# Kernel tuning notes

Hardware: AMD Instinct MI355X
Metric: run time of the kernel (lower is better)

The kernel has to match this reference:

```python
import jax, jax.numpy as jnp
import numpy as np

Lx, Ly, D, B = 6, 6, 3, 16
SIGMA = 0.5  # keeps the 36-tensor contraction magnitude in fp32 range


def _slice_config(T, s):
    # T: [Lx, Ly, D,D,D,D, 2,2,2,2,2]; bond axes (u,d,l,r), phys axes (self, up, down, left, right)
    sg = s.reshape(Lx, Ly)
    sp = jnp.pad(sg, 1)  # out-of-grid neighbors -> index 0
    ix, iy = jnp.meshgrid(jnp.arange(Lx), jnp.arange(Ly), indexing='ij')
    p = sg
    pu = sp[ix, iy + 1]      # neighbor (x-1, y)
    pd = sp[ix + 2, iy + 1]  # neighbor (x+1, y)
    pl = sp[ix + 1, iy]      # neighbor (x, y-1)
    pr = sp[ix + 1, iy + 2]  # neighbor (x, y+1)
    # advanced indexing: result [Lx, Ly, D, D, D, D] with bond axes (u, d, l, r)
    return T[ix, iy, :, :, :, :, p, pu, pd, pl, pr]


def _amplitude(T, s):
    # exact boundary contraction from ymin (no truncation), equals full .contract()
    A = _slice_config(T, s)            # [Lx, Ly, u, d, l, r]
    Bnd = A[:, 0, :, :, 0, :]          # cap dangling left bonds: [Lx, u, d, r]
    for y in range(1, Ly):
        C = A[:, y]                    # [Lx, u, d, l, r]
        Bnd = jnp.einsum('xabl,xudlr->xaubdr', Bnd, C)
        Bnd = Bnd.reshape(Lx, Bnd.shape[1] * Bnd.shape[2],
                          Bnd.shape[3] * Bnd.shape[4], D)
    M = Bnd[:, :, :, 0]                # cap dangling right bonds: [Lx, chi, chi]
    v = M[0, 0]                        # cap top boundary bond (index 0 of product bond)
    for xx in range(1, Lx):
        v = v @ M[xx]                  # vector-matrix chain down the boundary MPS
    return v[0]                        # cap bottom boundary bond


def setup_inputs() -> dict:
    key = jax.random.key(0)
    kT, kx = jax.random.split(key)
    T = jax.random.normal(kT, (Lx, Ly, D, D, D, D, 2, 2, 2, 2, 2), dtype=jnp.float32) * SIGMA
    x = jax.random.randint(kx, (B, Lx * Ly), 0, 2, dtype=jnp.int32)
    return {"x": x, "T": T}


def reference(x, T):
    # batched amplitudes: [B]
    return jax.vmap(lambda s: _amplitude(T, s))(x)
```

## Files before the change

kernel.cpp:

```cpp
#include <hip/hip_runtime.h>


constexpr int SITE_STRIDE = 81 * 32;

__global__ __launch_bounds__(512)
void peps_amp_kernel(const int* __restrict__ xs, const float* __restrict__ T,
                     float* __restrict__ out) {
    __shared__ float A[36 * 81];
    __shared__ float Vsh[2][729];
    __shared__ float Wsh[2][2][2187];
    __shared__ float red[8];
    __shared__ int sg[36];
    __shared__ int sidx[36];

    const int b = blockIdx.x;
    const int t = threadIdx.x;
    const int half = t >> 8;
    const int lt = t & 255;

    if (t < 36) sg[t] = xs[b * 36 + t];
    __syncthreads();
    if (t < 36) {
        const int i = t / 6, j = t % 6;
        const int p  = sg[t];
        const int pu = (i > 0) ? sg[t - 6] : 0;
        const int pd = (i < 5) ? sg[t + 6] : 0;
        const int pl = (j > 0) ? sg[t - 1] : 0;
        const int pr = (j < 5) ? sg[t + 1] : 0;
        sidx[t] = (((p * 2 + pu) * 2 + pd) * 2 + pl) * 2 + pr;
    }
    __syncthreads();
    for (int idx = t; idx < 36 * 81; idx += 512) {
        const int site = idx / 81;
        const int perm = idx - site * 81;
        A[idx] = T[site * SITE_STRIDE + perm * 32 + sidx[site]];
    }
    __syncthreads();

    float* V  = Vsh[half];
    float* Wa = Wsh[half][0];
    float* Wb = Wsh[half][1];
    const int SS = half ? 9 : 27;
    const int SO = half ? 27 : 9;

    {
        const float* Arow = &A[(half ? 30 : 0) * 81];
        for (int k = lt; k < 729; k += 256) {
            int c[6];
            c[0] = k / 243;
            c[1] = (k / 81) % 3;
            c[2] = (k / 27) % 3;
            c[3] = (k / 9) % 3;
            c[4] = (k / 3) % 3;
            c[5] = k % 3;
            float v0 = Arow[c[0] * SO + 0];
            float v1 = Arow[c[0] * SO + 1];
            float v2 = Arow[c[0] * SO + 2];
            #pragma unroll
            for (int y = 1; y <= 4; ++y) {
                const float* Ay = Arow + y * 81 + c[y] * SO;
                const float n0 = v0 * Ay[0] + v1 * Ay[3] + v2 * Ay[6];
                const float n1 = v0 * Ay[1] + v1 * Ay[4] + v2 * Ay[7];
                const float n2 = v0 * Ay[2] + v1 * Ay[5] + v2 * Ay[8];
                v0 = n0; v1 = n1; v2 = n2;
            }
            const float* A5 = Arow + 5 * 81 + c[5] * SO;
            V[k] = v0 * A5[0] + v1 * A5[3] + v2 * A5[6];
        }
    }
    __syncthreads();

    for (int cc = 0; cc < 2; ++cc) {
        const int xc = half ? (4 - cc) : (1 + cc);
        const float* Arow = &A[xc * 6 * 81];

        if (lt < 243) {
            const float v0 = V[lt], v1 = V[243 + lt], v2 = V[486 + lt];
            const float* A0 = Arow;
            #pragma unroll
            for (int o = 0; o < 3; ++o)
                #pragma unroll
                for (int r = 0; r < 3; ++r) {
                    Wa[(o * 3 + r) * 243 + lt] =
                        v0 * A0[o * SO + r] +
                        v1 * A0[SS + o * SO + r] +
                        v2 * A0[2 * SS + o * SO + r];
                }
        }
        __syncthreads();

        int cur = 0;
        int P = 81;
        #pragma unroll
        for (int y = 1; y <= 4; ++y) {
            const float* Ay = Arow + y * 81;
            const float* Wp = cur ? Wb : Wa;
            float* Wn = cur ? Wa : Wb;
            if (lt < 243) {
                const int dc = lt / P;
                const int ur = lt - dc * P;
                float wv[3][3];
                #pragma unroll
                for (int l = 0; l < 3; ++l)
                    #pragma unroll
                    for (int s = 0; s < 3; ++s)
                        wv[s][l] = Wp[(dc * 3 + l) * 3 * P + s * P + ur];
                #pragma unroll
                for (int o = 0; o < 3; ++o)
                    #pragma unroll
                    for (int r = 0; r < 3; ++r) {
                        float acc = 0.f;
                        #pragma unroll
                        for (int s = 0; s < 3; ++s)
                            #pragma unroll
                            for (int l = 0; l < 3; ++l)
                                acc += wv[s][l] * Ay[s * SS + o * SO + l * 3 + r];
                        Wn[((dc * 3 + o) * 3 + r) * P + ur] = acc;
                    }
            }
            __syncthreads();
            cur ^= 1;
            P /= 3;
        }

        {
            const float* Ay = Arow + 5 * 81;
            const float* Wp = cur ? Wb : Wa;
            if (lt < 243) {
                float wv[3][3];
                #pragma unroll
                for (int l = 0; l < 3; ++l)
                    #pragma unroll
                    for (int s = 0; s < 3; ++s)
                        wv[s][l] = Wp[(lt * 3 + l) * 3 + s];
                #pragma unroll
                for (int o = 0; o < 3; ++o) {
                    float acc = 0.f;
                    #pragma unroll
                    for (int s = 0; s < 3; ++s)
                        #pragma unroll
                        for (int l = 0; l < 3; ++l)
                            acc += wv[s][l] * Ay[s * SS + o * SO + l * 3];
                    V[lt * 3 + o] = acc;
                }
            }
        }
        __syncthreads();
    }

    float partial = 0.f;
    for (int i = t; i < 729; i += 512) partial += Vsh[0][i] * Vsh[1][i];
    #pragma unroll
    for (int off = 32; off > 0; off >>= 1) partial += __shfl_down(partial, off);
    if ((t & 63) == 0) red[t >> 6] = partial;
    __syncthreads();
    if (t == 0) {
        float s = 0.f;
        #pragma unroll
        for (int w = 0; w < 8; ++w) s += red[w];
        out[b] = s;
    }
}

extern "C" void kernel_launch(void* const* d_in, const int* in_sizes, int n_in,
                              void* d_out, int out_size, void* d_ws, size_t ws_size,
                              hipStream_t stream) {
    const int* xs = (const int*)d_in[0];
    const float* T = (const float*)d_in[1];
    float* out = (float*)d_out;
    const int B = in_sizes[0] / 36;
    peps_amp_kernel<<<B, 512, 0, stream>>>(xs, T, out);
}
```

Before: 68.49 us.

## Precontract column sites into two halves and apply each column as two matmuls

Replaces the per-site sequential boundary sweep over each column (five synchronized steps per column) with precomputed partial contractions. Sites 0-2 and sites 3-5 of each column are folded into two 2187-element operators G and B, built in one parallel pass alongside the initial boundary vector. Each column update then becomes two small matrix products (V through G into F, then F through B back into V), cutting barriers per column from about six to two. The cost is several times more shared memory (likely lowering occupancy) and redundant FLOPs in building G and B. It also reads the spin neighbors straight from global memory, dropping one barrier.

```diff
diff --git a/kernel.cpp b/kernel.cpp
--- a/kernel.cpp
+++ b/kernel.cpp
@@ -8,9 +8,12 @@
                      float* __restrict__ out) {
     __shared__ float A[36 * 81];
     __shared__ float Vsh[2][729];
-    __shared__ float Wsh[2][2][2187];
+    __shared__ float Gsh[2][2][2187];
+    __shared__ float Bsh[2][2][2187];
+    __shared__ float Fsh[2][2187];
+    __shared__ float T01sh[2][2][243];
+    __shared__ float T45sh[2][2][243];
     __shared__ float red[8];
-    __shared__ int sg[36];
     __shared__ int sidx[36];
 
     const int b = blockIdx.x;
@@ -18,15 +21,14 @@
     const int half = t >> 8;
     const int lt = t & 255;
 
-    if (t < 36) sg[t] = xs[b * 36 + t];
-    __syncthreads();
     if (t < 36) {
         const int i = t / 6, j = t % 6;
-        const int p  = sg[t];
-        const int pu = (i > 0) ? sg[t - 6] : 0;
-        const int pd = (i < 5) ? sg[t + 6] : 0;
-        const int pl = (j > 0) ? sg[t - 1] : 0;
-        const int pr = (j < 5) ? sg[t + 1] : 0;
+        const int base = b * 36;
+        const int p  = xs[base + t];
+        const int pu = (i > 0) ? xs[base + t - 6] : 0;
+        const int pd = (i < 5) ? xs[base + t + 6] : 0;
+        const int pl = (j > 0) ? xs[base + t - 1] : 0;
+        const int pr = (j < 5) ? xs[base + t + 1] : 0;
         sidx[t] = (((p * 2 + pu) * 2 + pd) * 2 + pl) * 2 + pr;
     }
     __syncthreads();
@@ -37,113 +39,140 @@
     }
     __syncthreads();
 
-    float* V  = Vsh[half];
-    float* Wa = Wsh[half][0];
-    float* Wb = Wsh[half][1];
     const int SS = half ? 9 : 27;
     const int SO = half ? 27 : 9;
 
     {
-        const float* Arow = &A[(half ? 30 : 0) * 81];
-        for (int k = lt; k < 729; k += 256) {
-            int c[6];
-            c[0] = k / 243;
-            c[1] = (k / 81) % 3;
-            c[2] = (k / 27) % 3;
-            c[3] = (k / 9) % 3;
-            c[4] = (k / 3) % 3;
-            c[5] = k % 3;
-            float v0 = Arow[c[0] * SO + 0];
-            float v1 = Arow[c[0] * SO + 1];
-            float v2 = Arow[c[0] * SO + 2];
-            #pragma unroll
-            for (int y = 1; y <= 4; ++y) {
-                const float* Ay = Arow + y * 81 + c[y] * SO;
-                const float n0 = v0 * Ay[0] + v1 * Ay[3] + v2 * Ay[6];
-                const float n1 = v0 * Ay[1] + v1 * Ay[4] + v2 * Ay[7];
-                const float n2 = v0 * Ay[2] + v1 * Ay[5] + v2 * Ay[8];
-                v0 = n0; v1 = n1; v2 = n2;
+        const float* Ab = &A[(half ? 30 : 0) * 81];
+        for (int idx = lt; idx < 1701; idx += 256) {
+            if (idx < 729) {
+                const int k = idx;
+                const int c0 = k / 243, c1 = (k / 81) % 3, c2 = (k / 27) % 3;
+                const int c3 = (k / 9) % 3, c4 = (k / 3) % 3, c5 = k % 3;
+                float v0 = Ab[c0 * SO + 0];
+                float v1 = Ab[c0 * SO + 1];
+                float v2 = Ab[c0 * SO + 2];
+                const float* P1p = Ab + 81 + c1 * SO;
+                float n0 = v0 * P1p[0] + v1 * P1p[3] + v2 * P1p[6];
+                float n1 = v0 * P1p[1] + v1 * P1p[4] + v2 * P1p[7];
+                float n2 = v0 * P1p[2] + v1 * P1p[5] + v2 * P1p[8];
+                const float* P2p = Ab + 162 + c2 * SO;
+                v0 = n0 * P2p[0] + n1 * P2p[3] + n2 * P2p[6];
+                v1 = n0 * P2p[1] + n1 * P2p[4] + n2 * P2p[7];
+                v2 = n0 * P2p[2] + n1 * P2p[5] + n2 * P2p[8];
+                const float* P3p = Ab + 243 + c3 * SO;
+                n0 = v0 * P3p[0] + v1 * P3p[3] + v2 * P3p[6];
+                n1 = v0 * P3p[1] + v1 * P3p[4] + v2 * P3p[7];
+                n2 = v0 * P3p[2] + v1 * P3p[5] + v2 * P3p[8];
+                const float* P4p = Ab + 324 + c4 * SO;
+                v0 = n0 * P4p[0] + n1 * P4p[3] + n2 * P4p[6];
+                v1 = n0 * P4p[1] + n1 * P4p[4] + n2 * P4p[7];
+                v2 = n0 * P4p[2] + n1 * P4p[5] + n2 * P4p[8];
+                const float* P5p = Ab + 405 + c5 * SO;
+                Vsh[half][k] = v0 * P5p[0] + v1 * P5p[3] + v2 * P5p[6];
+            } else if (idx < 729 + 486) {
+                int e = idx - 729;
+                const int c = e / 243; e -= c * 243;
+                const int u01 = e / 27, o01 = (e / 3) % 9, b2 = e % 3;
+                const int u0 = u01 / 3, u1 = u01 % 3, o0 = o01 / 3, o1 = o01 % 3;
+                const float* Ar = &A[(half ? (4 - c) : (1 + c)) * 486];
+                float acc = 0.f;
+                #pragma unroll
+                for (int b1 = 0; b1 < 3; ++b1)
+                    acc += Ar[u0 * SS + o0 * SO + b1] *
+                           Ar[81 + u1 * SS + o1 * SO + b1 * 3 + b2];
+                T01sh[half][c][e] = acc;
+            } else {
+                int e = idx - 729 - 486;
+                const int c = e / 243; e -= c * 243;
+                const int u45 = e / 27, o45 = (e / 3) % 9, b4 = e % 3;
+                const int u4 = u45 / 3, u5 = u45 % 3, o4 = o45 / 3, o5 = o45 % 3;
+                const float* Ar = &A[(half ? (4 - c) : (1 + c)) * 486];
+                float acc = 0.f;
+                #pragma unroll
+                for (int b5 = 0; b5 < 3; ++b5)
+                    acc += Ar[324 + u4 * SS + o4 * SO + b4 * 3 + b5] *
+                           Ar[405 + u5 * SS + o5 * SO + b5 * 3];
+                T45sh[half][c][e] = acc;
             }
-            const float* A5 = Arow + 5 * 81 + c[5] * SO;
-            V[k] = v0 * A5[0] + v1 * A5[3] + v2 * A5[6];
-        }
-    }
-    __syncthreads();
-
-    for (int cc = 0; cc < 2; ++cc) {
-        const int xc = half ? (4 - cc) : (1 + cc);
-        const float* Arow = &A[xc * 6 * 81];
+        }
+    }
+    __syncthreads();
+
+    for (int idx = lt; idx < 8748; idx += 256) {
+        const int c = idx / 4374;
+        int rem = idx - c * 4374;
+        const int isB = rem / 2187;
+        const int e = rem - isB * 2187;
+        const int oc = e / 81, g = (e / 27) % 3, uc = e % 27;
+        const float* Ar = &A[(half ? (4 - c) : (1 + c)) * 486];
+        float acc = 0.f;
+        if (!isB) {
+            const int o01 = oc / 3, o2 = oc % 3, u01 = uc / 3, u2 = uc % 3;
+            const float* t01 = &T01sh[half][c][u01 * 27 + o01 * 3];
+            const float* a2 = &Ar[162 + u2 * SS + o2 * SO];
+            #pragma unroll
+            for (int b2 = 0; b2 < 3; ++b2)
+                acc += t01[b2] * a2[b2 * 3 + g];
+            Gsh[half][c][e] = acc;
+        } else {
+            const int o3 = oc / 9, o45 = oc % 9, u3 = uc / 9, u45 = uc % 9;
+            const float* a3 = &Ar[243 + u3 * SS + o3 * SO + g * 3];
+            const float* t45 = &T45sh[half][c][u45 * 27 + o45 * 3];
+            #pragma unroll
+            for (int b4 = 0; b4 < 3; ++b4)
+                acc += a3[b4] * t45[b4];
+            Bsh[half][c][e] = acc;
+        }
+    }
+    __syncthreads();
+
+    for (int c = 0; c < 2; ++c) {
+        const float* G = Gsh[half][c];
+        const float* Bt = Bsh[half][c];
+        float* F = Fsh[half];
+        float* V = Vsh[half];
 
         if (lt < 243) {
-            const float v0 = V[lt], v1 = V[243 + lt], v2 = V[486 + lt];
-            const float* A0 = Arow;
-            #pragma unroll
-            for (int o = 0; o < 3; ++o)
-                #pragma unroll
-                for (int r = 0; r < 3; ++r) {
-                    Wa[(o * 3 + r) * 243 + lt] =
-                        v0 * A0[o * SO + r] +
-                        v1 * A0[SS + o * SO + r] +
-                        v2 * A0[2 * SS + o * SO + r];
-                }
+            const int oc = lt / 9;
+            const int gk = lt - oc * 9;
+            const int g = gk / 3, k = gk - g * 3;
+            float acc[9] = {0, 0, 0, 0, 0, 0, 0, 0, 0};
+            const float* Grow = &G[oc * 81 + g * 27];
+            #pragma unroll
+            for (int u = 0; u < 27; ++u) {
+                const float gv = Grow[u];
+                const float* vp = &V[u * 27 + k * 9];
+                #pragma unroll
+                for (int m = 0; m < 9; ++m) acc[m] += gv * vp[m];
+            }
+            float* Fp = &F[oc * 81 + g * 27 + k * 9];
+            #pragma unroll
+            for (int m = 0; m < 9; ++m) Fp[m] = acc[m];
         }
         __syncthreads();
 
-        int cur = 0;
-        int P = 81;
-        #pragma unroll
-        for (int y = 1; y <= 4; ++y) {
-            const float* Ay = Arow + y * 81;
-            const float* Wp = cur ? Wb : Wa;
-            float* Wn = cur ? Wa : Wb;
-            if (lt < 243) {
-                const int dc = lt / P;
-                const int ur = lt - dc * P;
-                float wv[3][3];
-                #pragma unroll
-                for (int l = 0; l < 3; ++l)
-                    #pragma unroll
-                    for (int s = 0; s < 3; ++s)
-                        wv[s][l] = Wp[(dc * 3 + l) * 3 * P + s * P + ur];
-                #pragma unroll
-                for (int o = 0; o < 3; ++o)
-                    #pragma unroll
-                    for (int r = 0; r < 3; ++r) {
-                        float acc = 0.f;
-                        #pragma unroll
-                        for (int s = 0; s < 3; ++s)
-                            #pragma unroll
-                            for (int l = 0; l < 3; ++l)
-                                acc += wv[s][l] * Ay[s * SS + o * SO + l * 3 + r];
-                        Wn[((dc * 3 + o) * 3 + r) * P + ur] = acc;
-                    }
-            }
-            __syncthreads();
-            cur ^= 1;
-            P /= 3;
-        }
-
-        {
-            const float* Ay = Arow + 5 * 81;
-            const float* Wp = cur ? Wb : Wa;
-            if (lt < 243) {
-                float wv[3][3];
-                #pragma unroll
-                for (int l = 0; l < 3; ++l)
-                    #pragma unroll
-                    for (int s = 0; s < 3; ++s)
-                        wv[s][l] = Wp[(lt * 3 + l) * 3 + s];
-                #pragma unroll
-                for (int o = 0; o < 3; ++o) {
-                    float acc = 0.f;
-                    #pragma unroll
-                    for (int s = 0; s < 3; ++s)
-                        #pragma unroll
-                        for (int l = 0; l < 3; ++l)
-                            acc += wv[s][l] * Ay[s * SS + o * SO + l * 3];
-                    V[lt * 3 + o] = acc;
+        if (lt < 243) {
+            const int oc = lt / 9;
+            const int q = lt - oc * 9;
+            float a0 = 0.f, a1 = 0.f, a2v = 0.f;
+            #pragma unroll
+            for (int g = 0; g < 3; ++g) {
+                const float* Fp = &F[oc * 81 + g * 27];
+                const float* B0 = &Bt[(q * 3 + 0) * 81 + g * 27];
+                const float* B1 = &Bt[(q * 3 + 1) * 81 + g * 27];
+                const float* B2 = &Bt[(q * 3 + 2) * 81 + g * 27];
+                #pragma unroll
+                for (int u = 0; u < 27; ++u) {
+                    const float fv = Fp[u];
+                    a0 += fv * B0[u];
+                    a1 += fv * B1[u];
+                    a2v += fv * B2[u];
                 }
             }
+            V[oc * 27 + q * 3 + 0] = a0;
+            V[oc * 27 + q * 3 + 1] = a1;
+            V[oc * 27 + q * 3 + 2] = a2v;
         }
         __syncthreads();
     }
```

After: 80.91 us. +18.1%, slower.

## Fuse column contraction steps pairwise and precompute boundary pair products

Applied to the files above, without the earlier changes.

Each thread now computes the site index directly from global memory, which removes two setup barriers. The kernel precomputes products of adjacent boundary-row site pairs while loading A, so the first boundary vector is built from three pair matrices instead of six chained site steps. Interior column sweeps fuse two site contractions per thread with registers holding the intermediate, halving the number of barriers and shared-memory round trips. The cost is redundant sidx computation per element and higher register pressure in the fused step.

```diff
diff --git a/kernel.cpp b/kernel.cpp
--- a/kernel.cpp
+++ b/kernel.cpp
@@ -2,6 +2,64 @@
 
 
 constexpr int SITE_STRIDE = 81 * 32;
+
+__device__ __forceinline__ int calc_sidx(const int* __restrict__ xs, int base, int s) {
+    const int i = s / 6, j = s - (s / 6) * 6;
+    const int p  = xs[base + s];
+    const int pu = (i > 0) ? xs[base + s - 6] : 0;
+    const int pd = (i < 5) ? xs[base + s + 6] : 0;
+    const int pl = (j > 0) ? xs[base + s - 1] : 0;
+    const int pr = (j < 5) ? xs[base + s + 1] : 0;
+    return (((p * 2 + pu) * 2 + pd) * 2 + pl) * 2 + pr;
+}
+
+template <int U>
+__device__ __forceinline__ void fused2(int lt, const float* __restrict__ Win,
+                                       float* __restrict__ Wout,
+                                       const float* __restrict__ A1,
+                                       const float* __restrict__ A2,
+                                       int SS, int SO) {
+    if (lt >= 243) return;
+    const int D  = lt / (3 * U);
+    const int rem = lt - D * 3 * U;
+    const int o1 = rem / U;
+    const int ur = rem - o1 * U;
+    const float* Wb = Win + D * 27 * U + ur;
+    float win[3][3][3];
+    #pragma unroll
+    for (int l = 0; l < 3; ++l)
+        #pragma unroll
+        for (int s = 0; s < 3; ++s)
+            #pragma unroll
+            for (int m = 0; m < 3; ++m)
+                win[l][s][m] = Wb[((l * 9 + s * 3 + m) * U)];
+    float tt[3][3];
+    #pragma unroll
+    for (int r1 = 0; r1 < 3; ++r1)
+        #pragma unroll
+        for (int m = 0; m < 3; ++m) {
+            float acc = 0.f;
+            #pragma unroll
+            for (int s = 0; s < 3; ++s)
+                #pragma unroll
+                for (int l = 0; l < 3; ++l)
+                    acc += win[l][s][m] * A1[s * SS + o1 * SO + l * 3 + r1];
+            tt[r1][m] = acc;
+        }
+    float* Wo = Wout + (D * 3 + o1) * 9 * U + ur;
+    #pragma unroll
+    for (int o2 = 0; o2 < 3; ++o2)
+        #pragma unroll
+        for (int r2 = 0; r2 < 3; ++r2) {
+            float acc = 0.f;
+            #pragma unroll
+            for (int m = 0; m < 3; ++m)
+                #pragma unroll
+                for (int r1 = 0; r1 < 3; ++r1)
+                    acc += tt[r1][m] * A2[m * SS + o2 * SO + r1 * 3 + r2];
+            Wo[(o2 * 3 + r2) * U] = acc;
+        }
+}
 
 __global__ __launch_bounds__(512)
 void peps_amp_kernel(const int* __restrict__ xs, const float* __restrict__ T,
@@ -9,70 +67,69 @@
     __shared__ float A[36 * 81];
     __shared__ float Vsh[2][729];
     __shared__ float Wsh[2][2][2187];
+    __shared__ float Pm[2][3][81];
     __shared__ float red[8];
-    __shared__ int sg[36];
-    __shared__ int sidx[36];
 
     const int b = blockIdx.x;
     const int t = threadIdx.x;
     const int half = t >> 8;
     const int lt = t & 255;
+    const int base = b * 36;
 
-    if (t < 36) sg[t] = xs[b * 36 + t];
-    __syncthreads();
-    if (t < 36) {
-        const int i = t / 6, j = t % 6;
-        const int p  = sg[t];
-        const int pu = (i > 0) ? sg[t - 6] : 0;
-        const int pd = (i < 5) ? sg[t + 6] : 0;
-        const int pl = (j > 0) ? sg[t - 1] : 0;
-        const int pr = (j < 5) ? sg[t + 1] : 0;
-        sidx[t] = (((p * 2 + pu) * 2 + pd) * 2 + pl) * 2 + pr;
-    }
-    __syncthreads();
-    for (int idx = t; idx < 36 * 81; idx += 512) {
-        const int site = idx / 81;
-        const int perm = idx - site * 81;
-        A[idx] = T[site * SITE_STRIDE + perm * 32 + sidx[site]];
+    for (int idx = t; idx < 2916 + 486; idx += 512) {
+        if (idx < 2916) {
+            const int site = idx / 81;
+            const int perm = idx - site * 81;
+            A[idx] = T[site * SITE_STRIDE + perm * 32 + calc_sidx(xs, base, site)];
+        } else {
+            const int e = idx - 2916;
+            const int ph = e / 243;
+            const int rem = e - ph * 243;
+            const int p = rem / 81;
+            const int q = rem - p * 81;
+            const int cc2 = q / 9, lr = q - cc2 * 9;
+            const int ca = cc2 / 3, cb = cc2 - ca * 3;
+            const int l = lr / 3, r = lr - l * 3;
+            const int SOh = ph ? 27 : 9;
+            const int sa = (ph ? 30 : 0) + 2 * p;
+            const int sb = sa + 1;
+            const int sxa = calc_sidx(xs, base, sa);
+            const int sxb = calc_sidx(xs, base, sb);
+            const float* Ta = T + sa * SITE_STRIDE + sxa;
+            const float* Tb = T + sb * SITE_STRIDE + sxb;
+            float acc = 0.f;
+            #pragma unroll
+            for (int m = 0; m < 3; ++m)
+                acc += Ta[(ca * SOh + l * 3 + m) * 32] *
+                       Tb[(cb * SOh + m * 3 + r) * 32];
+            Pm[ph][p][q] = acc;
+        }
     }
     __syncthreads();
 
+    const int SS = half ? 9 : 27;
+    const int SO = half ? 27 : 9;
     float* V  = Vsh[half];
     float* Wa = Wsh[half][0];
     float* Wb = Wsh[half][1];
-    const int SS = half ? 9 : 27;
-    const int SO = half ? 27 : 9;
 
-    {
-        const float* Arow = &A[(half ? 30 : 0) * 81];
-        for (int k = lt; k < 729; k += 256) {
-            int c[6];
-            c[0] = k / 243;
-            c[1] = (k / 81) % 3;
-            c[2] = (k / 27) % 3;
-            c[3] = (k / 9) % 3;
-            c[4] = (k / 3) % 3;
-            c[5] = k % 3;
-            float v0 = Arow[c[0] * SO + 0];
-            float v1 = Arow[c[0] * SO + 1];
-            float v2 = Arow[c[0] * SO + 2];
-            #pragma unroll
-            for (int y = 1; y <= 4; ++y) {
-                const float* Ay = Arow + y * 81 + c[y] * SO;
-                const float n0 = v0 * Ay[0] + v1 * Ay[3] + v2 * Ay[6];
-                const float n1 = v0 * Ay[1] + v1 * Ay[4] + v2 * Ay[7];
-                const float n2 = v0 * Ay[2] + v1 * Ay[5] + v2 * Ay[8];
-                v0 = n0; v1 = n1; v2 = n2;
-            }
-            const float* A5 = Arow + 5 * 81 + c[5] * SO;
-            V[k] = v0 * A5[0] + v1 * A5[3] + v2 * A5[6];
-        }
+    for (int k = lt; k < 729; k += 256) {
+        const int c01 = k / 81;
+        const int c23 = (k / 9) % 9;
+        const int c45 = k % 9;
+        const float* p0 = &Pm[half][0][c01 * 9];
+        const float* p1 = &Pm[half][1][c23 * 9];
+        const float* p2 = &Pm[half][2][c45 * 9];
+        float w0 = p0[0] * p1[0] + p0[1] * p1[3] + p0[2] * p1[6];
+        float w1 = p0[0] * p1[1] + p0[1] * p1[4] + p0[2] * p1[7];
+        float w2 = p0[0] * p1[2] + p0[1] * p1[5] + p0[2] * p1[8];
+        V[k] = w0 * p2[0] + w1 * p2[3] + w2 * p2[6];
     }
     __syncthreads();
 
     for (int cc = 0; cc < 2; ++cc) {
         const int xc = half ? (4 - cc) : (1 + cc);
-        const float* Arow = &A[xc * 6 * 81];
+        const float* Arow = &A[xc * 486];
 
         if (lt < 243) {
             const float v0 = V[lt], v1 = V[243 + lt], v2 = V[486 + lt];
@@ -89,60 +146,28 @@
         }
         __syncthreads();
 
-        int cur = 0;
-        int P = 81;
-        #pragma unroll
-        for (int y = 1; y <= 4; ++y) {
-            const float* Ay = Arow + y * 81;
-            const float* Wp = cur ? Wb : Wa;
-            float* Wn = cur ? Wa : Wb;
-            if (lt < 243) {
-                const int dc = lt / P;
-                const int ur = lt - dc * P;
-                float wv[3][3];
+        fused2<27>(lt, Wa, Wb, Arow + 81, Arow + 162, SS, SO);
+        __syncthreads();
+        fused2<3>(lt, Wb, Wa, Arow + 243, Arow + 324, SS, SO);
+        __syncthreads();
+
+        if (lt < 243) {
+            const float* Ay = Arow + 405;
+            float wv[3][3];
+            #pragma unroll
+            for (int l = 0; l < 3; ++l)
                 #pragma unroll
-                for (int l = 0; l < 3; ++l)
+                for (int s = 0; s < 3; ++s)
+                    wv[s][l] = Wa[(lt * 3 + l) * 3 + s];
+            #pragma unroll
+            for (int o = 0; o < 3; ++o) {
+                float acc = 0.f;
+                #pragma unroll
+                for (int s = 0; s < 3; ++s)
                     #pragma unroll
-                    for (int s = 0; s < 3; ++s)
-                        wv[s][l] = Wp[(dc * 3 + l) * 3 * P + s * P + ur];
-                #pragma unroll
-                for (int o = 0; o < 3; ++o)
-                    #pragma unroll
-                    for (int r = 0; r < 3; ++r) {
-                        float acc = 0.f;
-                        #pragma unroll
-                        for (int s = 0; s < 3; ++s)
-                            #pragma unroll
-                            for (int l = 0; l < 3; ++l)
-                                acc += wv[s][l] * Ay[s * SS + o * SO + l * 3 + r];
-                        Wn[((dc * 3 + o) * 3 + r) * P + ur] = acc;
-                    }
-            }
-            __syncthreads();
-            cur ^= 1;
-            P /= 3;
-        }
-
-        {
-            const float* Ay = Arow + 5 * 81;
-            const float* Wp = cur ? Wb : Wa;
-            if (lt < 243) {
-                float wv[3][3];
-                #pragma unroll
-                for (int l = 0; l < 3; ++l)
-                    #pragma unroll
-                    for (int s = 0; s < 3; ++s)
-                        wv[s][l] = Wp[(lt * 3 + l) * 3 + s];
-                #pragma unroll
-                for (int o = 0; o < 3; ++o) {
-                    float acc = 0.f;
-                    #pragma unroll
-                    for (int s = 0; s < 3; ++s)
-                        #pragma unroll
-                        for (int l = 0; l < 3; ++l)
-                            acc += wv[s][l] * Ay[s * SS + o * SO + l * 3];
-                    V[lt * 3 + o] = acc;
-                }
+                    for (int l = 0; l < 3; ++l)
+                        acc += wv[s][l] * Ay[s * SS + o * SO + l * 3];
+                V[lt * 3 + o] = acc;
             }
         }
         __syncthreads();
```

After: 71.66 us. 1.05x slower.
